# Performance work log

Measured on AMD Instinct MI355X. Metric: run time of the kernel, lower is better.

The kernel has to match this reference:

```python
import jax, jax.numpy as jnp
import numpy as np

_SAMPLING_EPS = 1e-05
_RMAX = 0.9999999403953552          # largest float32 uniform from tl.rand
_RMAX_LOG = -5.960464477539063e-08  # log(_RMAX)


def setup_inputs() -> dict:
    key = jax.random.key(0)
    k1, k2, k3, k4, k5 = jax.random.split(key, 5)
    B, V = 256, 128000
    logits = jax.random.normal(k1, (B, V), dtype=jnp.float32) * 4.0
    temperature = jax.random.uniform(k2, (B,), dtype=jnp.float32, minval=0.1, maxval=1.5)
    top_k = jax.random.randint(k3, (B,), 1, 1000).astype(jnp.int32)
    top_p = jax.random.uniform(k4, (B,), dtype=jnp.float32, minval=0.5, maxval=1.0)
    gumbel_u = jax.random.uniform(k5, (B, V), dtype=jnp.float32)
    return {
        "logits": logits,
        "temperature": temperature,
        "top_k": top_k,
        "top_p": top_p,
        "gumbel_u": gumbel_u,
        "num_logprobs": 20,
    }


def reference(logits, temperature, top_k, top_p, gumbel_u, num_logprobs):
    B, V = logits.shape
    # --- apply_temperature: divide by temp, temp<eps treated as 1.0 (greedy) ---
    temp = jnp.where(temperature < _SAMPLING_EPS, 1.0, temperature)
    logits = logits.astype(jnp.float32) / temp[:, None]

    # --- apply_top_k_top_p: sort ascending, mask, scatter back ---
    idx_sort = jnp.argsort(logits, axis=-1)                      # ascending
    logits_sort = jnp.take_along_axis(logits, idx_sort, axis=-1)
    # top-k: value of the k-th largest is at position V-k in ascending order
    k_pos = (V - top_k.astype(jnp.int32))[:, None]
    thresh = jnp.take_along_axis(logits_sort, k_pos, axis=-1)    # [B,1]
    logits_sort = jnp.where(logits_sort < thresh, -jnp.inf, logits_sort)
    # top-p: drop ascending prefix whose cumulative prob <= 1-p (keep last)
    probs_sort = jax.nn.softmax(logits_sort, axis=-1)
    cum = jnp.cumsum(probs_sort, axis=-1)
    mask_p = cum <= (1.0 - top_p)[:, None]
    mask_p = mask_p.at[:, -1].set(False)
    logits_sort = jnp.where(mask_p, -jnp.inf, logits_sort)
    # unsort back to vocab order
    inv = jnp.argsort(idx_sort, axis=-1)
    logits_f = jnp.take_along_axis(logits_sort, inv, axis=-1)

    # --- softmax + gumbel-trick sampling: argmax(p / -log(u)) ---
    probs = jax.nn.softmax(logits_f, axis=-1)
    q = -jnp.where(gumbel_u >= _RMAX, _RMAX_LOG, jnp.log(gumbel_u))
    greedy = (temperature < _SAMPLING_EPS)[:, None]  # kernel skips these rows
    ratio = jnp.where(greedy, probs, probs / q)
    sampled = jnp.argmax(ratio, axis=-1)             # [B]

    # --- gather_logprobs ---
    logprobs = jax.nn.log_softmax(logits_f, axis=-1)
    sampled_lp = jnp.take_along_axis(logprobs, sampled[:, None], axis=-1)  # [B,1]
    ranks = jnp.sum(logprobs > sampled_lp, axis=-1)                        # [B]
    topk_lp, topk_idx = jax.lax.top_k(logprobs, num_logprobs)
    indices = jnp.concatenate([sampled[:, None], topk_idx], axis=1)        # [B,1+K]
    lp_vals = jnp.concatenate([sampled_lp, topk_lp], axis=1)               # [B,1+K]

    return sampled[:, None], indices, lp_vals, ranks
```

## Files before the change

### kernel.cpp

```cpp
#include <hip/hip_runtime.h>
#include <math.h>

#define NTHR 1024
#define CAP 4096
#define BINS 4096
#define SMALL 1024
#define GUARD 16u

#define RMAX_F 0.9999999403953552f
#define RMAX_LOG_F -5.960464477539063e-08f
#define NEG_BIG -3.0e38f

__device__ __forceinline__ unsigned keyOf(float v) {
    unsigned b = __float_as_uint(v);
    return (b & 0x80000000u) ? ~b : (b | 0x80000000u);
}
__device__ __forceinline__ float valOfKey(unsigned k) {
    unsigned b = (k & 0x80000000u) ? (k ^ 0x80000000u) : ~k;
    return __uint_as_float(b);
}
__device__ __forceinline__ unsigned long long shflXor64(unsigned long long v, int m) {
    int lo = __shfl_xor((int)(unsigned)v, m);
    int hi = __shfl_xor((int)(unsigned)(v >> 32), m);
    return ((unsigned long long)(unsigned)hi << 32) | (unsigned)lo;
}

__global__ __launch_bounds__(NTHR) void sampler_kernel(
    const float* __restrict__ logits,
    const float* __restrict__ temperature,
    const int* __restrict__ top_kv,
    const float* __restrict__ top_pv,
    const float* __restrict__ gumbel,
    float* __restrict__ out,
    int B, int V, int K)
{
    const int r = blockIdx.x;
    const int tid = threadIdx.x;
    const int lane = tid & 63;
    const int wid = tid >> 6;

    __shared__ unsigned long long cand[CAP];
    __shared__ unsigned long long cand2[SMALL];
    __shared__ unsigned refHist[512];
    __shared__ int wtotI[16];
    __shared__ float varr[1024];
    __shared__ float Earr[1024];
    __shared__ float sfx[1024];
    __shared__ unsigned char flagArr[1024];
    __shared__ unsigned bitmap[64];
    __shared__ unsigned s_prefix;
    __shared__ int s_cntgt, s_total, s_lvl;
    __shared__ int s_ncand, s_nc2, s_nkeep, s_rank, s_g0, s_g1;
    __shared__ unsigned long long s_amax;
    __shared__ float s_vs;

    unsigned* hist = (unsigned*)cand;

    const float* row = logits + (long long)r * V;
    const float* urow = gumbel + (long long)r * V;

    float traw = temperature[r];
    bool greedy = traw < 1e-5f;
    float t = greedy ? 1.0f : traw;
    int k = top_kv[r];
    if (k < 1) k = 1;
    if (k > V) k = V;
    float p = top_pv[r];

    const float4* row4 = (const float4*)row;
    const int V4 = V >> 2;
    const int Vt = V4 << 2;
    const unsigned cpy = tid & 1u;

    for (int i = tid; i < BINS * 2; i += NTHR) hist[i] = 0;
    __syncthreads();
#define H4(v4) do { \
        atomicAdd(&hist[((keyOf((v4).x) >> 20) << 1) | cpy], 1u); \
        atomicAdd(&hist[((keyOf((v4).y) >> 20) << 1) | cpy], 1u); \
        atomicAdd(&hist[((keyOf((v4).z) >> 20) << 1) | cpy], 1u); \
        atomicAdd(&hist[((keyOf((v4).w) >> 20) << 1) | cpy], 1u); \
    } while (0)
    {
        int i = tid;
        for (; i + 3 * NTHR < V4; i += 4 * NTHR) {
            float4 a = row4[i];
            float4 b = row4[i + NTHR];
            float4 c = row4[i + 2 * NTHR];
            float4 d = row4[i + 3 * NTHR];
            H4(a); H4(b); H4(c); H4(d);
        }
        for (; i < V4; i += NTHR) {
            float4 a = row4[i];
            H4(a);
        }
        for (int ii = Vt + tid; ii < V; ii += NTHR)
            atomicAdd(&hist[((keyOf(row[ii]) >> 20) << 1) | cpy], 1u);
    }
    __syncthreads();
    {
        int base = tid << 2;
        int cs = 0;
        #pragma unroll
        for (int j = 0; j < 4; ++j)
            cs += (int)(hist[(base + j) * 2] + hist[(base + j) * 2 + 1]);
        int vv = cs;
        #pragma unroll
        for (int d = 1; d < 64; d <<= 1) {
            int o = __shfl_down(vv, d);
            if (lane + d < 64) vv += o;
        }
        if (lane == 0) wtotI[wid] = vv;
        __syncthreads();
        int off = 0;
        for (int w = wid + 1; w < 16; ++w) off += wtotI[w];
        int mine = vv + off;
        int above = mine - cs;
        if (mine >= k && above < k) {
            int run = above;
            for (int b = base + 3; b >= base; --b) {
                int mb = (int)(hist[b * 2] + hist[b * 2 + 1]);
                if (run + mb >= k) {
                    s_prefix = (unsigned)b; s_cntgt = run; s_total = run + mb; s_lvl = 0;
                    break;
                }
                run += mb;
            }
        }
    }
    for (int level = 1; level <= 2; ++level) {
        __syncthreads();
        if (s_total <= CAP) break;
        for (int i = tid; i < 512; i += NTHR) hist[i] = 0;
        __syncthreads();
        unsigned pfx = s_prefix;
        const int msh = 32 - (12 + 8 * (level - 1));
        const int bsh = msh - 8;
        for (int i = tid; i < V4; i += NTHR) {
            float4 l4 = row4[i];
            float vv[4] = { l4.x, l4.y, l4.z, l4.w };
            #pragma unroll
            for (int j = 0; j < 4; ++j) {
                unsigned key = keyOf(vv[j]);
                if ((key >> msh) == pfx)
                    atomicAdd(&hist[(((key >> bsh) & 255u) << 1) | cpy], 1u);
            }
        }
        for (int i = Vt + tid; i < V; i += NTHR) {
            unsigned key = keyOf(row[i]);
            if ((key >> msh) == pfx)
                atomicAdd(&hist[(((key >> bsh) & 255u) << 1) | cpy], 1u);
        }
        __syncthreads();
        if (tid == 0) {
            int run = s_cntgt;
            for (int b = 255; b >= 0; --b) {
                int mb = (int)(hist[b * 2] + hist[b * 2 + 1]);
                if (run + mb >= k) {
                    s_prefix = (pfx << 8) | (unsigned)b; s_cntgt = run; s_total = run + mb;
                    break;
                }
                run += mb;
            }
            s_lvl = level;
        }
    }
    __syncthreads();
    const unsigned tlo = s_prefix << (20 - 8 * s_lvl);
    const float thrF = valOfKey(tlo);
    if (tid == 0) s_ncand = 0;
    __syncthreads();

#define EMIT_CAND(val, gidx_) do { \
        bool pred = ((val) >= thrF); \
        unsigned long long mask = __ballot(pred ? 1 : 0); \
        if (mask) { \
            int leader = __ffsll(mask) - 1; \
            int cnt = __popcll(mask); \
            int bpos = 0; \
            if (lane == leader) bpos = atomicAdd(&s_ncand, cnt); \
            bpos = __shfl(bpos, leader); \
            if (pred) { \
                int pos = bpos + __popcll(mask & ((1ULL << lane) - 1ULL)); \
                if (pos < CAP) { \
                    unsigned key = keyOf(val); \
                    cand[pos] = ((unsigned long long)key << 32) | (unsigned)(~(gidx_)); \
                } \
            } \
        } \
    } while (0)
#define C4(v4, i4) do { \
        EMIT_CAND((v4).x, (unsigned)((i4) * 4 + 0)); \
        EMIT_CAND((v4).y, (unsigned)((i4) * 4 + 1)); \
        EMIT_CAND((v4).z, (unsigned)((i4) * 4 + 2)); \
        EMIT_CAND((v4).w, (unsigned)((i4) * 4 + 3)); \
    } while (0)
    {
        int i = tid;
        for (; i + 3 * NTHR < V4; i += 4 * NTHR) {
            float4 a = row4[i];
            float4 b = row4[i + NTHR];
            float4 c = row4[i + 2 * NTHR];
            float4 d = row4[i + 3 * NTHR];
            C4(a, i); C4(b, i + NTHR); C4(c, i + 2 * NTHR); C4(d, i + 3 * NTHR);
        }
        for (; i < V4; i += NTHR) {
            float4 a = row4[i];
            C4(a, i);
        }
        for (int ii = Vt + tid; ii < V; ii += NTHR) {
            float lv = row[ii];
            EMIT_CAND(lv, (unsigned)ii);
        }
    }
    __syncthreads();
    int ncand = s_ncand; if (ncand > CAP) ncand = CAP;
    if (k > ncand) k = ncand;

    bool fromC2 = false;
    bool bigSort = false;
    if (ncand > SMALL) {
        unsigned pfx = s_prefix;
        int run = s_cntgt;
        int bb = 20 - 8 * s_lvl;
        while (bb > 0) {
            int step = (bb >= 8) ? 8 : bb;
            bb -= step;
            int nbins = 1 << step;
            for (int i = tid; i < nbins * 2; i += NTHR) refHist[i] = 0;
            __syncthreads();
            for (int i = tid; i < ncand; i += NTHR) {
                unsigned key = (unsigned)(cand[i] >> 32);
                if ((key >> (bb + step)) == pfx)
                    atomicAdd(&refHist[(((key >> bb) & (unsigned)(nbins - 1)) << 1) | cpy], 1u);
            }
            __syncthreads();
            int cnt = 0;
            if (tid < 256) cnt = (tid < nbins) ? (int)(refHist[tid * 2] + refHist[tid * 2 + 1]) : 0;
            int vv = cnt;
            #pragma unroll
            for (int d = 1; d < 64; d <<= 1) {
                int o = __shfl_down(vv, d);
                if (lane + d < 64) vv += o;
            }
            if (tid < 256 && lane == 0) wtotI[wid] = vv;
            __syncthreads();
            if (tid < 256) {
                int off = 0;
                for (int w = wid + 1; w < 4; ++w) off += wtotI[w];
                int incl = vv + off;
                int abv = incl - cnt;
                int kk = k - run;
                if (incl >= kk && abv < kk) {
                    s_prefix = (pfx << step) | (unsigned)tid;
                    s_cntgt = run + abv;
                }
            }
            __syncthreads();
            pfx = s_prefix;
            run = s_cntgt;
        }
        unsigned tref = (pfx >= tlo + GUARD) ? (pfx - GUARD) : tlo;
        if (tid == 0) s_nc2 = 0;
        __syncthreads();
        for (int i = tid; i < ncand; i += NTHR) {
            unsigned long long cv = cand[i];
            bool pred = ((unsigned)(cv >> 32) >= tref);
            unsigned long long mask = __ballot(pred ? 1 : 0);
            if (mask) {
                int leader = __ffsll(mask) - 1;
                int cnt2 = __popcll(mask);
                int bpos = 0;
                if (lane == leader) bpos = atomicAdd(&s_nc2, cnt2);
                bpos = __shfl(bpos, leader);
                if (pred) {
                    int pos = bpos + __popcll(mask & ((1ULL << lane) - 1ULL));
                    if (pos < SMALL) cand2[pos] = cv;
                }
            }
        }
        __syncthreads();
        int nc2 = s_nc2;
        if (nc2 <= SMALL) { ncand = nc2; fromC2 = true; }
        else bigSort = true;
    }

    unsigned long long vreg = 0ULL;
    if (!bigSort) {
        const unsigned long long* src = fromC2 ? cand2 : cand;
        unsigned long long v = (tid < ncand) ? src[tid] : 0ULL;
        #pragma unroll
        for (int size = 2; size <= SMALL; size <<= 1) {
            #pragma unroll
            for (int stride = size >> 1; stride > 0; stride >>= 1) {
                unsigned long long o;
                if (stride < 64) {
                    o = shflXor64(v, stride);
                } else {
                    cand[tid] = v;
                    __syncthreads();
                    o = cand[tid ^ stride];
                    __syncthreads();
                }
                bool takeMax = (((tid & size) == 0) == ((tid & stride) == 0));
                unsigned long long mx = (v > o) ? v : o;
                unsigned long long mn = (v > o) ? o : v;
                v = takeMax ? mx : mn;
            }
        }
        cand[tid] = v;
        vreg = v;
        varr[tid] = (tid < ncand) ? (valOfKey((unsigned)(vreg >> 32)) / t) : NEG_BIG;
        __syncthreads();
    } else {
        int P = 2; while (P < ncand) P <<= 1;
        for (int i = ncand + tid; i < P; i += NTHR) cand[i] = 0ULL;
        __syncthreads();
        for (int size = 2; size <= P; size <<= 1) {
            for (int stride = size >> 1; stride > 0; stride >>= 1) {
                for (int i = tid; i < P; i += NTHR) {
                    int j = i ^ stride;
                    if (j > i) {
                        unsigned long long a = cand[i], b = cand[j];
                        bool up = ((i & size) == 0);
                        bool sw = up ? (a < b) : (a > b);
                        if (sw) { cand[i] = b; cand[j] = a; }
                    }
                }
                __syncthreads();
            }
        }
        for (int i = tid; i < 1024; i += NTHR)
            varr[i] = (i < ncand) ? (valOfKey((unsigned)(cand[i] >> 32)) / t) : NEG_BIG;
        __syncthreads();
    }

    const float m = varr[0];
    const float tkeyV = varr[k - 1];
    int ntop = k;
    while (ntop < ncand) {
        float vi = (ntop < 1024) ? varr[ntop]
                                 : (valOfKey((unsigned)(cand[ntop] >> 32)) / t);
        if (vi != tkeyV) break;
        ++ntop;
    }
    if (ntop > 1024) ntop = 1024;

    {
        float e = (tid < ntop) ? expf(varr[tid] - m) : 0.0f;
        Earr[tid] = e;
        sfx[tid] = e;
    }
    __syncthreads();
    for (int d = 1; d < 1024; d <<= 1) {
        float t0 = (tid + d < 1024) ? sfx[tid + d] : 0.0f;
        __syncthreads();
        sfx[tid] += t0;
        __syncthreads();
    }
    const float Zp = sfx[0];
    const float cmp = 1.0f - p;
    if (tid == 0) { s_nkeep = 0; s_rank = 0; s_amax = 0ULL; }
    for (int i = tid; i < 64; i += NTHR) bitmap[i] = 0;
    __syncthreads();
    {
        int local = 0;
        for (int i = tid; i < ntop; i += NTHR)
            if (sfx[i] / Zp > cmp) local++;
        #pragma unroll
        for (int d = 1; d < 64; d <<= 1) local += __shfl_xor(local, d);
        if (lane == 0 && local) atomicAdd(&s_nkeep, local);
    }
    __syncthreads();
    const int nkeep = s_nkeep;
    if (tid == 0) {
        float vb = varr[nkeep - 1];
        int g0 = nkeep - 1;
        while (g0 > 0 && varr[g0 - 1] == vb) --g0;
        int g1 = nkeep;
        while (g1 < ntop && varr[g1] == vb) ++g1;
        s_g0 = g0; s_g1 = g1;
    }
    __syncthreads();
    const int g0 = s_g0, g1 = s_g1;
    const int mkeep = nkeep - g0;
    for (int i = g0 + tid; i < g1; i += NTHR) {
        unsigned gi = ~(unsigned)(cand[i] & 0xFFFFFFFFull);
        int rk = 0;
        for (int j = g0; j < g1; ++j) {
            unsigned gj = ~(unsigned)(cand[j] & 0xFFFFFFFFull);
            if (gj > gi) rk++;
        }
        flagArr[i] = (rk < mkeep) ? 1 : 0;
    }
    __syncthreads();

    const float Z2 = (nkeep < 1024) ? (Zp - sfx[nkeep]) : Zp;
    const float L = logf(Z2);

    {
        unsigned long long lm = 0ULL;
        for (int i = tid; i < g1; i += NTHR) {
            if (i < g0 || flagArr[i]) {
                unsigned lo = (unsigned)(cand[i] & 0xFFFFFFFFull);
                unsigned gidx = ~lo;
                float u = urow[gidx];
                float q = -((u >= RMAX_F) ? RMAX_LOG_F : logf(u));
                float prob = Earr[i] / Z2;
                float ratio = greedy ? prob : (prob / q);
                unsigned long long comp = ((unsigned long long)__float_as_uint(ratio) << 32) | lo;
                if (comp > lm) lm = comp;
                if (gidx < 2048) atomicOr(&bitmap[gidx >> 5], 1u << (gidx & 31));
            }
        }
        #pragma unroll
        for (int d = 1; d < 64; d <<= 1) {
            unsigned long long o = shflXor64(lm, d);
            if (o > lm) lm = o;
        }
        if (lane == 0 && lm) atomicMax(&s_amax, lm);
    }
    __syncthreads();
    const unsigned samp_lo = (unsigned)(s_amax & 0xFFFFFFFFull);
    const unsigned samp = ~samp_lo;
    for (int i = tid; i < ntop; i += NTHR)
        if ((unsigned)(cand[i] & 0xFFFFFFFFull) == samp_lo) s_vs = varr[i];
    __syncthreads();
    const float lp_s = (s_vs - m) - L;
    {
        int local = 0;
        for (int i = tid; i < nkeep; i += NTHR)
            if ((varr[i] - m) - L > lp_s) local++;
        #pragma unroll
        for (int d = 1; d < 64; d <<= 1) local += __shfl_xor(local, d);
        if (lane == 0 && local) atomicAdd(&s_rank, local);
    }
    __syncthreads();

    float* o_samp = out;
    float* o_idx  = out + B;
    float* o_lp   = out + B + (long long)B * (K + 1);
    float* o_rank = out + B + 2LL * B * (K + 1);
    const long long rowo = (long long)r * (K + 1);
    const int ntk = (nkeep < K) ? nkeep : K;

    if (tid < g1) {
        const int i = tid;
        bool kept = (i < g0) || flagArr[i];
        if (kept) {
            float v = varr[i];
            int rs, re, base;
            if (i >= g0) { rs = g0; re = g1; base = g0; }
            else {
                rs = i; while (rs > 0 && varr[rs - 1] == v) --rs;
                re = i + 1; while (re < g1 && varr[re] == v) ++re;
                base = rs;
            }
            if (base < ntk) {
                unsigned myidx = ~(unsigned)(cand[i] & 0xFFFFFFFFull);
                int cnt = 0;
                for (int j = rs; j < re; ++j) {
                    if (j == i) continue;
                    if (j >= g0 && !flagArr[j]) continue;
                    unsigned gj = ~(unsigned)(cand[j] & 0xFFFFFFFFull);
                    if (gj < myidx) cnt++;
                }
                int slot = base + cnt;
                if (slot < ntk) {
                    o_idx[rowo + 1 + slot] = (float)myidx;
                    o_lp[rowo + 1 + slot] = (v - m) - L;
                }
            }
        }
    }

    if (tid == 0) {
        o_samp[r] = (float)samp;
        o_idx[rowo] = (float)samp;
        o_lp[rowo] = lp_s;
        o_rank[r] = (float)s_rank;
        if (nkeep < K) {
            int j = 0;
            for (int c = nkeep; c < K; ++c) {
                while (bitmap[j >> 5] & (1u << (j & 31))) ++j;
                o_idx[rowo + 1 + c] = (float)j;
                o_lp[rowo + 1 + c] = NEG_BIG;
                ++j;
            }
        }
    }
}

extern "C" void kernel_launch(void* const* d_in, const int* in_sizes, int n_in,
                              void* d_out, int out_size, void* d_ws, size_t ws_size,
                              hipStream_t stream) {
    const float* logits      = (const float*)d_in[0];
    const float* temperature = (const float*)d_in[1];
    const int*   top_k       = (const int*)d_in[2];
    const float* top_p       = (const float*)d_in[3];
    const float* gumbel      = (const float*)d_in[4];
    int B = in_sizes[1];
    int V = in_sizes[0] / B;
    int K = (out_size / B - 4) / 2;
    sampler_kernel<<<B, NTHR, 0, stream>>>(logits, temperature, top_k, top_p,
                                           gumbel, (float*)d_out, B, V, K);
}
```

Baseline: 281.2 us.

## Estimate top-k threshold from sampled histogram and skip full histogram pass

Builds a coarse histogram from one float4 per thread, a sample of 4096 of the row's 128000 values, and picks a conservative threshold targeting about 3k+500 candidates. It then collects candidates in a single pass over the row using per-thread shared atomics. If the count is below k or above the enlarged CAP, it falls back to the original exact histogram path. This is meant to remove a full-row histogram pass over the logits, at the cost of a larger candidate buffer, an extra radix refinement over 32 bits of candidates, and heavier contention on the shared counter.

Result: faster. 268.0 us (-4.7%).

```diff
diff --git a/kernel.cpp b/kernel.cpp
--- a/kernel.cpp
+++ b/kernel.cpp
@@ -2,10 +2,11 @@
 #include <math.h>
 
 #define NTHR 1024
-#define CAP 4096
+#define CAP 8192
 #define BINS 4096
 #define SMALL 1024
 #define GUARD 16u
+#define SS 4096
 
 #define RMAX_F 0.9999999403953552f
 #define RMAX_LOG_F -5.960464477539063e-08f
@@ -72,31 +73,37 @@
     const int Vt = V4 << 2;
     const unsigned cpy = tid & 1u;
 
-    for (int i = tid; i < BINS * 2; i += NTHR) hist[i] = 0;
-    __syncthreads();
 #define H4(v4) do { \
         atomicAdd(&hist[((keyOf((v4).x) >> 20) << 1) | cpy], 1u); \
         atomicAdd(&hist[((keyOf((v4).y) >> 20) << 1) | cpy], 1u); \
         atomicAdd(&hist[((keyOf((v4).z) >> 20) << 1) | cpy], 1u); \
         atomicAdd(&hist[((keyOf((v4).w) >> 20) << 1) | cpy], 1u); \
     } while (0)
-    {
-        int i = tid;
-        for (; i + 3 * NTHR < V4; i += 4 * NTHR) {
-            float4 a = row4[i];
-            float4 b = row4[i + NTHR];
-            float4 c = row4[i + 2 * NTHR];
-            float4 d = row4[i + 3 * NTHR];
-            H4(a); H4(b); H4(c); H4(d);
-        }
-        for (; i < V4; i += NTHR) {
-            float4 a = row4[i];
-            H4(a);
-        }
-        for (int ii = Vt + tid; ii < V; ii += NTHR)
-            atomicAdd(&hist[((keyOf(row[ii]) >> 20) << 1) | cpy], 1u);
-    }
-    __syncthreads();
+#define SPEC1(val, gidx_, thr_) do { \
+        float _v = (val); \
+        if (_v >= (thr_)) { \
+            int _pos = atomicAdd(&s_ncand, 1); \
+            if (_pos < CAP) \
+                cand[_pos] = ((unsigned long long)keyOf(_v) << 32) | (unsigned)(~(unsigned)(gidx_)); \
+        } \
+    } while (0)
+
+    for (int i = tid; i < BINS * 2; i += NTHR) hist[i] = 0;
+    __syncthreads();
+    {
+        int f4pos = (int)(((long long)tid * V4) >> 10);
+        float4 sv = row4[f4pos];
+        H4(sv);
+    }
+    __syncthreads();
+    int ts;
+    {
+        int tc = 3 * k + 500;
+        if (tc > 3500) tc = 3500;
+        if (tc < 700) tc = 700;
+        ts = (int)(((long long)tc * SS + V - 1) / V);
+        if (ts < 4) ts = 4;
+    }
     {
         int base = tid << 2;
         int cs = 0;
@@ -115,85 +122,20 @@
         for (int w = wid + 1; w < 16; ++w) off += wtotI[w];
         int mine = vv + off;
         int above = mine - cs;
-        if (mine >= k && above < k) {
+        if (mine >= ts && above < ts) {
             int run = above;
             for (int b = base + 3; b >= base; --b) {
                 int mb = (int)(hist[b * 2] + hist[b * 2 + 1]);
-                if (run + mb >= k) {
-                    s_prefix = (unsigned)b; s_cntgt = run; s_total = run + mb; s_lvl = 0;
-                    break;
-                }
+                if (run + mb >= ts) { s_prefix = (unsigned)b; break; }
                 run += mb;
             }
         }
-    }
-    for (int level = 1; level <= 2; ++level) {
-        __syncthreads();
-        if (s_total <= CAP) break;
-        for (int i = tid; i < 512; i += NTHR) hist[i] = 0;
-        __syncthreads();
-        unsigned pfx = s_prefix;
-        const int msh = 32 - (12 + 8 * (level - 1));
-        const int bsh = msh - 8;
-        for (int i = tid; i < V4; i += NTHR) {
-            float4 l4 = row4[i];
-            float vv[4] = { l4.x, l4.y, l4.z, l4.w };
-            #pragma unroll
-            for (int j = 0; j < 4; ++j) {
-                unsigned key = keyOf(vv[j]);
-                if ((key >> msh) == pfx)
-                    atomicAdd(&hist[(((key >> bsh) & 255u) << 1) | cpy], 1u);
-            }
-        }
-        for (int i = Vt + tid; i < V; i += NTHR) {
-            unsigned key = keyOf(row[i]);
-            if ((key >> msh) == pfx)
-                atomicAdd(&hist[(((key >> bsh) & 255u) << 1) | cpy], 1u);
-        }
-        __syncthreads();
-        if (tid == 0) {
-            int run = s_cntgt;
-            for (int b = 255; b >= 0; --b) {
-                int mb = (int)(hist[b * 2] + hist[b * 2 + 1]);
-                if (run + mb >= k) {
-                    s_prefix = (pfx << 8) | (unsigned)b; s_cntgt = run; s_total = run + mb;
-                    break;
-                }
-                run += mb;
-            }
-            s_lvl = level;
-        }
-    }
-    __syncthreads();
-    const unsigned tlo = s_prefix << (20 - 8 * s_lvl);
-    const float thrF = valOfKey(tlo);
-    if (tid == 0) s_ncand = 0;
-    __syncthreads();
-
-#define EMIT_CAND(val, gidx_) do { \
-        bool pred = ((val) >= thrF); \
-        unsigned long long mask = __ballot(pred ? 1 : 0); \
-        if (mask) { \
-            int leader = __ffsll(mask) - 1; \
-            int cnt = __popcll(mask); \
-            int bpos = 0; \
-            if (lane == leader) bpos = atomicAdd(&s_ncand, cnt); \
-            bpos = __shfl(bpos, leader); \
-            if (pred) { \
-                int pos = bpos + __popcll(mask & ((1ULL << lane) - 1ULL)); \
-                if (pos < CAP) { \
-                    unsigned key = keyOf(val); \
-                    cand[pos] = ((unsigned long long)key << 32) | (unsigned)(~(gidx_)); \
-                } \
-            } \
-        } \
-    } while (0)
-#define C4(v4, i4) do { \
-        EMIT_CAND((v4).x, (unsigned)((i4) * 4 + 0)); \
-        EMIT_CAND((v4).y, (unsigned)((i4) * 4 + 1)); \
-        EMIT_CAND((v4).z, (unsigned)((i4) * 4 + 2)); \
-        EMIT_CAND((v4).w, (unsigned)((i4) * 4 + 3)); \
-    } while (0)
+        if (tid == 0) s_ncand = 0;
+        __syncthreads();
+    }
+    unsigned tlo = s_prefix << 20;
+    float thrF = valOfKey(tlo);
+
     {
         int i = tid;
         for (; i + 3 * NTHR < V4; i += 4 * NTHR) {
@@ -201,37 +143,167 @@
             float4 b = row4[i + NTHR];
             float4 c = row4[i + 2 * NTHR];
             float4 d = row4[i + 3 * NTHR];
-            C4(a, i); C4(b, i + NTHR); C4(c, i + 2 * NTHR); C4(d, i + 3 * NTHR);
+            SPEC1(a.x, i * 4 + 0, thrF); SPEC1(a.y, i * 4 + 1, thrF);
+            SPEC1(a.z, i * 4 + 2, thrF); SPEC1(a.w, i * 4 + 3, thrF);
+            SPEC1(b.x, (i + NTHR) * 4 + 0, thrF); SPEC1(b.y, (i + NTHR) * 4 + 1, thrF);
+            SPEC1(b.z, (i + NTHR) * 4 + 2, thrF); SPEC1(b.w, (i + NTHR) * 4 + 3, thrF);
+            SPEC1(c.x, (i + 2 * NTHR) * 4 + 0, thrF); SPEC1(c.y, (i + 2 * NTHR) * 4 + 1, thrF);
+            SPEC1(c.z, (i + 2 * NTHR) * 4 + 2, thrF); SPEC1(c.w, (i + 2 * NTHR) * 4 + 3, thrF);
+            SPEC1(d.x, (i + 3 * NTHR) * 4 + 0, thrF); SPEC1(d.y, (i + 3 * NTHR) * 4 + 1, thrF);
+            SPEC1(d.z, (i + 3 * NTHR) * 4 + 2, thrF); SPEC1(d.w, (i + 3 * NTHR) * 4 + 3, thrF);
         }
         for (; i < V4; i += NTHR) {
             float4 a = row4[i];
-            C4(a, i);
-        }
-        for (int ii = Vt + tid; ii < V; ii += NTHR) {
-            float lv = row[ii];
-            EMIT_CAND(lv, (unsigned)ii);
-        }
-    }
-    __syncthreads();
-    int ncand = s_ncand; if (ncand > CAP) ncand = CAP;
+            SPEC1(a.x, i * 4 + 0, thrF); SPEC1(a.y, i * 4 + 1, thrF);
+            SPEC1(a.z, i * 4 + 2, thrF); SPEC1(a.w, i * 4 + 3, thrF);
+        }
+        for (int ii = Vt + tid; ii < V; ii += NTHR)
+            SPEC1(row[ii], ii, thrF);
+    }
+    __syncthreads();
+    int ncand = s_ncand;
+    const bool fastok = (ncand >= k && ncand <= CAP);
+
+    if (!fastok) {
+        for (int i = tid; i < BINS * 2; i += NTHR) hist[i] = 0;
+        __syncthreads();
+        {
+            int i = tid;
+            for (; i + 3 * NTHR < V4; i += 4 * NTHR) {
+                float4 a = row4[i];
+                float4 b = row4[i + NTHR];
+                float4 c = row4[i + 2 * NTHR];
+                float4 d = row4[i + 3 * NTHR];
+                H4(a); H4(b); H4(c); H4(d);
+            }
+            for (; i < V4; i += NTHR) { float4 a = row4[i]; H4(a); }
+            for (int ii = Vt + tid; ii < V; ii += NTHR)
+                atomicAdd(&hist[((keyOf(row[ii]) >> 20) << 1) | cpy], 1u);
+        }
+        __syncthreads();
+        {
+            int base = tid << 2;
+            int cs = 0;
+            #pragma unroll
+            for (int j = 0; j < 4; ++j)
+                cs += (int)(hist[(base + j) * 2] + hist[(base + j) * 2 + 1]);
+            int vv = cs;
+            #pragma unroll
+            for (int d = 1; d < 64; d <<= 1) {
+                int o = __shfl_down(vv, d);
+                if (lane + d < 64) vv += o;
+            }
+            if (lane == 0) wtotI[wid] = vv;
+            __syncthreads();
+            int off = 0;
+            for (int w = wid + 1; w < 16; ++w) off += wtotI[w];
+            int mine = vv + off;
+            int above = mine - cs;
+            if (mine >= k && above < k) {
+                int run = above;
+                for (int b = base + 3; b >= base; --b) {
+                    int mb = (int)(hist[b * 2] + hist[b * 2 + 1]);
+                    if (run + mb >= k) {
+                        s_prefix = (unsigned)b; s_cntgt = run; s_total = run + mb; s_lvl = 0;
+                        break;
+                    }
+                    run += mb;
+                }
+            }
+        }
+        for (int level = 1; level <= 2; ++level) {
+            __syncthreads();
+            if (s_total <= CAP) break;
+            for (int i = tid; i < 512; i += NTHR) hist[i] = 0;
+            __syncthreads();
+            unsigned pfx = s_prefix;
+            const int msh = 32 - (12 + 8 * (level - 1));
+            const int bsh = msh - 8;
+            for (int i = tid; i < V4; i += NTHR) {
+                float4 l4 = row4[i];
+                float vv4[4] = { l4.x, l4.y, l4.z, l4.w };
+                #pragma unroll
+                for (int j = 0; j < 4; ++j) {
+                    unsigned key = keyOf(vv4[j]);
+                    if ((key >> msh) == pfx)
+                        atomicAdd(&hist[(((key >> bsh) & 255u) << 1) | cpy], 1u);
+                }
+            }
+            for (int i = Vt + tid; i < V; i += NTHR) {
+                unsigned key = keyOf(row[i]);
+                if ((key >> msh) == pfx)
+                    atomicAdd(&hist[(((key >> bsh) & 255u) << 1) | cpy], 1u);
+            }
+            __syncthreads();
+            if (tid == 0) {
+                int run = s_cntgt;
+                for (int b = 255; b >= 0; --b) {
+                    int mb = (int)(hist[b * 2] + hist[b * 2 + 1]);
+                    if (run + mb >= k) {
+                        s_prefix = (pfx << 8) | (unsigned)b; s_cntgt = run; s_total = run + mb;
+                        break;
+                    }
+                    run += mb;
+                }
+                s_lvl = level;
+            }
+        }
+        __syncthreads();
+        tlo = s_prefix << (20 - 8 * s_lvl);
+        thrF = valOfKey(tlo);
+        if (tid == 0) s_ncand = 0;
+        __syncthreads();
+        {
+            int i = tid;
+            for (; i + 3 * NTHR < V4; i += 4 * NTHR) {
+                float4 a = row4[i];
+                float4 b = row4[i + NTHR];
+                float4 c = row4[i + 2 * NTHR];
+                float4 d = row4[i + 3 * NTHR];
+                SPEC1(a.x, i * 4 + 0, thrF); SPEC1(a.y, i * 4 + 1, thrF);
+                SPEC1(a.z, i * 4 + 2, thrF); SPEC1(a.w, i * 4 + 3, thrF);
+                SPEC1(b.x, (i + NTHR) * 4 + 0, thrF); SPEC1(b.y, (i + NTHR) * 4 + 1, thrF);
+                SPEC1(b.z, (i + NTHR) * 4 + 2, thrF); SPEC1(b.w, (i + NTHR) * 4 + 3, thrF);
+                SPEC1(c.x, (i + 2 * NTHR) * 4 + 0, thrF); SPEC1(c.y, (i + 2 * NTHR) * 4 + 1, thrF);
+                SPEC1(c.z, (i + 2 * NTHR) * 4 + 2, thrF); SPEC1(c.w, (i + 2 * NTHR) * 4 + 3, thrF);
+                SPEC1(d.x, (i + 3 * NTHR) * 4 + 0, thrF); SPEC1(d.y, (i + 3 * NTHR) * 4 + 1, thrF);
+                SPEC1(d.z, (i + 3 * NTHR) * 4 + 2, thrF); SPEC1(d.w, (i + 3 * NTHR) * 4 + 3, thrF);
+            }
+            for (; i < V4; i += NTHR) {
+                float4 a = row4[i];
+                SPEC1(a.x, i * 4 + 0, thrF); SPEC1(a.y, i * 4 + 1, thrF);
+                SPEC1(a.z, i * 4 + 2, thrF); SPEC1(a.w, i * 4 + 3, thrF);
+            }
+            for (int ii = Vt + tid; ii < V; ii += NTHR)
+                SPEC1(row[ii], ii, thrF);
+        }
+        __syncthreads();
+        ncand = s_ncand;
+        if (ncand > CAP) ncand = CAP;
+        if (k > ncand) k = ncand;
+    }
     if (k > ncand) k = ncand;
 
     bool fromC2 = false;
     bool bigSort = false;
     if (ncand > SMALL) {
-        unsigned pfx = s_prefix;
-        int run = s_cntgt;
-        int bb = 20 - 8 * s_lvl;
+        unsigned pfx; int run; int bb;
+        if (fastok) { pfx = 0u; run = 0; bb = 32; }
+        else { pfx = s_prefix; run = s_cntgt; bb = 20 - 8 * s_lvl; }
         while (bb > 0) {
             int step = (bb >= 8) ? 8 : bb;
             bb -= step;
             int nbins = 1 << step;
             for (int i = tid; i < nbins * 2; i += NTHR) refHist[i] = 0;
             __syncthreads();
-            for (int i = tid; i < ncand; i += NTHR) {
-                unsigned key = (unsigned)(cand[i] >> 32);
-                if ((key >> (bb + step)) == pfx)
-                    atomicAdd(&refHist[(((key >> bb) & (unsigned)(nbins - 1)) << 1) | cpy], 1u);
+            {
+                int sh = bb + step;
+                for (int i = tid; i < ncand; i += NTHR) {
+                    unsigned key = (unsigned)(cand[i] >> 32);
+                    bool in = (sh >= 32) || ((key >> sh) == pfx);
+                    if (in)
+                        atomicAdd(&refHist[(((key >> bb) & (unsigned)(nbins - 1)) << 1) | cpy], 1u);
+                }
             }
             __syncthreads();
             int cnt = 0;
@@ -284,7 +356,6 @@
         else bigSort = true;
     }
 
-    unsigned long long vreg = 0ULL;
     if (!bigSort) {
         const unsigned long long* src = fromC2 ? cand2 : cand;
         unsigned long long v = (tid < ncand) ? src[tid] : 0ULL;
@@ -308,8 +379,7 @@
             }
         }
         cand[tid] = v;
-        vreg = v;
-        varr[tid] = (tid < ncand) ? (valOfKey((unsigned)(vreg >> 32)) / t) : NEG_BIG;
+        varr[tid] = (tid < ncand) ? (valOfKey((unsigned)(v >> 32)) / t) : NEG_BIG;
         __syncthreads();
     } else {
         int P = 2; while (P < ncand) P <<= 1;
```
